# Performance work log

Hardware: AMD Instinct MI355X
Metric: run time of the kernel (lower is better)

The kernel has to match this reference:

```python
import jax, jax.numpy as jnp
import numpy as np

N = 40000          # total samples; s pattern: first N//2 are group 0, rest group 1
TOP = 0.3          # top_percentile
LAM = 10.0
ITS = 10
P = 0.5


def setup_inputs() -> dict:
    key = jax.random.key(0)
    k1, k2 = jax.random.split(key)
    y_pred = jax.random.uniform(k1, (N,), dtype=jnp.float32)  # predicted probs in [0,1]
    # deterministic half/half sensitive attribute so group sizes are static
    s = (jnp.arange(N) >= N // 2).astype(jnp.int32)
    y_gt = jax.random.uniform(k2, (N,), dtype=jnp.float32)    # unused by forward math
    pct_a = jnp.full((1,), 0.2, dtype=jnp.float32)            # unused (threshold_based=False)
    pct_b = jnp.full((1,), 0.8, dtype=jnp.float32)            # unused
    return {"y_pred": y_pred, "s": s, "y_gt": y_gt, "pct_a": pct_a, "pct_b": pct_b}


def _wasserstein(y_pred):
    n = y_pred.shape[0]
    n0 = n // 2  # s==0 count (static: s is half zeros then half ones)
    y0 = y_pred[:n0]        # s == 0 group
    y1 = y_pred[n0:]        # s == 1 group
    nc = float(n0)
    nt = float(n - n0)
    # local_reg=True, threshold_based=False -> keep top `TOP` fraction after sort
    ia0 = int((1.0 - TOP) * n0)
    ia1 = int((1.0 - TOP) * (n - n0))
    y0 = jnp.sort(y0)[ia0:]  # (m0,)
    y1 = jnp.sort(y1)[ia1:]  # (m1,)
    m0 = y0.shape[0]
    m1 = y1.shape[0]
    # sqrt(cdist(.,p=2)**2) on 1-D points == |y1_i - y0_j|
    M = jnp.abs(y1[:, None] - y0[None, :])           # (m1, m0)
    delta = jax.lax.stop_gradient(jnp.max(M))
    eff_lam = jax.lax.stop_gradient(LAM / jnp.mean(M))
    # pad with slack row/col (delta cost, 0 in corner)
    row = delta * jnp.ones((1, m0), M.dtype)
    col = jnp.concatenate([delta * jnp.ones((m1, 1), M.dtype),
                           jnp.zeros((1, 1), M.dtype)], axis=0)
    Mt = jnp.concatenate([jnp.concatenate([M, row], axis=0), col], axis=1)  # (m1+1, m0+1)
    a = jnp.concatenate([P * jnp.ones((m1, 1), M.dtype) / nt,
                         (1.0 - P) * jnp.ones((1, 1), M.dtype)], axis=0)    # (m1+1, 1)
    b = jnp.concatenate([(1.0 - P) * jnp.ones((m0, 1), M.dtype) / nc,
                         P * jnp.ones((1, 1), M.dtype)], axis=0)            # (m0+1, 1)
    K = jnp.exp(-eff_lam * Mt) + 1e-6
    ainvK = K / a
    u = a
    for _ in range(ITS):  # fixed 10-step Sinkhorn fixed point
        u = 1.0 / (ainvK @ (b / (u.T @ K).T))
    v = b / (u.T @ K).T
    T = u * (v.T * K)
    T = jax.lax.stop_gradient(T)  # backpropT=False
    D = 2.0 * jnp.sum(T * Mt)
    return D


def reference(y_pred, s, y_gt, pct_a, pct_b):
    # s is the fixed half-zeros/half-ones pattern from setup_inputs; the static
    # slices in _wasserstein reproduce the original boolean masks exactly.
    reg_loss = _wasserstein(y_pred)
    z = jnp.zeros((1,), jnp.float32)
    return (reg_loss, z, z, z)
```

## Files before the change

kernel.cpp:

```cpp
#include <hip/hip_runtime.h>

#define HALF   20000
#define MSEL   6001
#define RANKLO 13999
#define NBUCK  4096
#define CANDMAX 8192

#define NTH   1024
#define TPT   6
#define NPAD  (NTH*TPT)

#define OFF_HIST   0
#define OFF_TSEL   8192
#define OFF_CCNT   8194
#define OFF_ZERO_N 8196
#define OFF_CANDV  8704
#define OFF_CANDI  25088
#define OFF_RANK   41472
#define OFF_XS     57856
#define OFF_YS     63872

#define LPREF 0
#define LSUFB 6144
#define LCX   12288
#define LCY   18432
#define LRED  24576
#define LSC   24640
#define SOLVE_LDS_FLOATS 24656
#define SOLVE_LDS_BYTES (SOLVE_LDS_FLOATS * 4)

__device__ __forceinline__ float fexp2(float x) {
#if defined(__has_builtin)
#if __has_builtin(__builtin_amdgcn_exp2f)
  return __builtin_amdgcn_exp2f(x);
#else
  return exp2f(x);
#endif
#else
  return exp2f(x);
#endif
}

__device__ __forceinline__ int bucket_of(float v) {
  int b = (int)(v * 4096.0f);
  b = b < 0 ? 0 : b;
  b = b > (NBUCK - 1) ? (NBUCK - 1) : b;
  return b;
}


__global__ __launch_bounds__(512) void k_zero(int* wsI) {
  int i = blockIdx.x * blockDim.x + threadIdx.x;
  if (i < OFF_ZERO_N) wsI[i] = 0;
  if (i < 2 * CANDMAX) wsI[OFF_RANK + i] = 0;
}

__global__ __launch_bounds__(512) void k_hist(const float* __restrict__ yp, int* wsI) {
  int i = blockIdx.x * blockDim.x + threadIdx.x;
  if (i >= 2 * HALF) return;
  int h = (i >= HALF) ? 1 : 0;
  atomicAdd(&wsI[OFF_HIST + h * NBUCK + bucket_of(yp[i])], 1);
}

__global__ __launch_bounds__(1024) void k_findt(int* wsI) {
  __shared__ int ss[1024];
  const int h = blockIdx.x;
  const int t = threadIdx.x;
  const int* hist = wsI + OFF_HIST + h * NBUCK;
  int c0 = hist[4 * t + 0], c1 = hist[4 * t + 1], c2 = hist[4 * t + 2], c3 = hist[4 * t + 3];
  ss[t] = c0 + c1 + c2 + c3;
  __syncthreads();
  for (int off = 1; off < 1024; off <<= 1) {
    int v = ss[t];
    if (t + off < 1024) v += ss[t + off];
    __syncthreads();
    ss[t] = v;
    __syncthreads();
  }
  int SSnext = (t < 1023) ? ss[t + 1] : 0;
  int R3 = c3 + SSnext;
  int R2 = c2 + R3;
  int R1 = c1 + R2;
  int R0 = c0 + R1;
  if (R0 >= MSEL && R1 < MSEL) wsI[OFF_TSEL + h] = 4 * t + 0;
  if (R1 >= MSEL && R2 < MSEL) wsI[OFF_TSEL + h] = 4 * t + 1;
  if (R2 >= MSEL && R3 < MSEL) wsI[OFF_TSEL + h] = 4 * t + 2;
  if (R3 >= MSEL && SSnext < MSEL) wsI[OFF_TSEL + h] = 4 * t + 3;
}

__global__ __launch_bounds__(512) void k_cand(const float* __restrict__ yp, int* wsI, float* wsF) {
  __shared__ int ss[512];
  __shared__ int sbase;
  const int h = blockIdx.y;
  const int tid = threadIdx.x;
  const int idx = blockIdx.x * 512 + tid;
  float v = 0.f;
  int flag = 0;
  if (idx < HALF) {
    v = yp[h * HALF + idx];
    flag = (bucket_of(v) >= wsI[OFF_TSEL + h]) ? 1 : 0;
  }
  ss[tid] = flag;
  __syncthreads();
  for (int off = 1; off < 512; off <<= 1) {
    int add = (tid >= off) ? ss[tid - off] : 0;
    __syncthreads();
    ss[tid] += add;
    __syncthreads();
  }
  if (tid == 511) sbase = atomicAdd(&wsI[OFF_CCNT + h], ss[511]);
  __syncthreads();
  if (flag) {
    int pos = sbase + ss[tid] - 1;
    if (pos < CANDMAX) {
      wsF[OFF_CANDV + h * CANDMAX + pos] = v;
      wsI[OFF_CANDI + h * CANDMAX + pos] = idx;
    }
  }
}

__global__ __launch_bounds__(512) void k_rankc(const int* __restrict__ wsIc, float* wsF, int* wsI) {
  __shared__ float cv[512];
  __shared__ int ci[512];
  const int h = blockIdx.z;
  const int tid = threadIdx.x;
  const int cnt = min(wsIc[OFF_CCNT + h], CANDMAX);
  const int cb = blockIdx.y * 512;
  if (cb >= cnt) return;
  const int clen = min(512, cnt - cb);
  if (tid < clen) {
    cv[tid] = wsF[OFF_CANDV + h * CANDMAX + cb + tid];
    ci[tid] = wsIc[OFF_CANDI + h * CANDMAX + cb + tid];
  }
  __syncthreads();
  const int g = blockIdx.x * 512 + tid;
  if (g >= cnt) return;
  const float v = wsF[OFF_CANDV + h * CANDMAX + g];
  const int li = wsIc[OFF_CANDI + h * CANDMAX + g];
  int r = 0;
  for (int l = 0; l < clen; ++l) {
    float w = cv[l];
    r += (w < v || (w == v && ci[l] < li)) ? 1 : 0;
  }
  atomicAdd(&wsI[OFF_RANK + h * CANDMAX + g], r);
}

__global__ __launch_bounds__(512) void k_place(const int* __restrict__ wsI, float* wsF) {
  const int h = blockIdx.y;
  const int g = blockIdx.x * 512 + threadIdx.x;
  const int cnt = min(wsI[OFF_CCNT + h], CANDMAX);
  if (g >= cnt) return;
  const int full = wsI[OFF_RANK + h * CANDMAX + g] + (HALF - cnt);
  if (full >= RANKLO) {
    wsF[(h ? OFF_YS : OFF_XS) + (full - RANKLO)] = wsF[OFF_CANDV + h * CANDMAX + g];
  }
}


__device__ __forceinline__ float block_reduce(float v, float* red) {
  const int tid = threadIdx.x;
  __syncthreads();
  for (int d = 1; d < 64; d <<= 1) v += __shfl_xor(v, d, 64);
  if ((tid & 63) == 0) red[tid >> 6] = v;
  __syncthreads();
  float r = 0.f;
  if (tid < 16) {
    r = red[tid];
    for (int d = 1; d < 16; d <<= 1) r += __shfl_xor(r, d, 16);
    if (tid == 0) red[0] = r;
  }
  __syncthreads();
  return red[0];
}

__device__ __forceinline__ int bsearch(const float* arr, float v) {
  int lo = 0, hi = MSEL;
  while (lo < hi) {
    int m = (lo + hi) >> 1;
    if (arr[m] <= v) lo = m + 1; else hi = m;
  }
  return lo;
}

__device__ __forceinline__ void scan_ab(const float (&a)[TPT], const float (&b)[TPT],
                                        float wsum, float* lds,
                                        int do_state, int sout, int lout, float lnext) {
  float* PrefA = lds + LPREF;
  float* SufB = lds + LSUFB;
  float* red = lds + LRED;
  float* scal = lds + LSC;
  const int tid = threadIdx.x;
  const int wv = tid >> 6, ln = tid & 63;
  float pa[TPT], sb[TPT];
  float ta = 0.f;
#pragma unroll
  for (int k = 0; k < TPT; ++k) { pa[k] = ta; ta += a[k]; }
  float tb = 0.f;
#pragma unroll
  for (int k = TPT - 1; k >= 0; --k) { tb += b[k]; sb[k] = tb; }
  float ia = ta, ib = tb, iw = wsum;
#pragma unroll
  for (int d = 1; d < 64; d <<= 1) {
    float oa = __shfl_up(ia, d, 64);
    float ob = __shfl_down(ib, d, 64);
    float ow = __shfl_xor(iw, d, 64);
    if (ln >= d) ia += oa;
    if (ln + d < 64) ib += ob;
    iw += ow;
  }
  if (ln == 63) red[wv] = ia;
  if (ln == 0) { red[16 + wv] = ib; red[32 + wv] = iw; }
  __syncthreads();
  if (tid < 16) {
    float wa = red[tid], wb = red[16 + tid], ww = red[32 + tid];
    float sa = wa, sbw = wb, sw = ww;
#pragma unroll
    for (int d = 1; d < 16; d <<= 1) {
      float oa = __shfl_up(sa, d, 16);
      float ob = __shfl_down(sbw, d, 16);
      float ow = __shfl_xor(sw, d, 16);
      if (tid >= d) sa += oa;
      if (tid + d < 16) sbw += ob;
      sw += ow;
    }
    red[tid] = sa - wa;
    red[16 + tid] = sbw - wb;
    if (tid == 15) red[48] = sa;
    if (tid == 0) {
      red[49] = sw;
      if (do_state) { scal[sout] = sw; scal[lout] = lnext; }
    }
  }
  __syncthreads();
  const float GA = red[wv] + (ia - ta);
  const float GB = red[16 + wv] + (ib - tb);
  const int base = tid * TPT;
#pragma unroll
  for (int k = 0; k < TPT; ++k) {
    PrefA[base + k] = GA + pa[k];
    SufB[base + k] = GB + sb[k];
  }
  __syncthreads();
}

__device__ __forceinline__ void do_pass(float* lds, const float* zin, float* zout,
                                        const float (&SA)[TPT], const float (&SB)[TPT],
                                        const float (&TA)[TPT], const float (&TB)[TPT],
                                        const int (&tp)[TPT],
                                        int mode, int sin, int lin, int sout, int lout) {
  float* PrefA = lds + LPREF;
  float* SufB = lds + LSUFB;
  float* scal = lds + LSC;
  const int tid = threadIdx.x;
  const int base = tid * TPT;
  const float au = 0.5f / 20000.0f;
  const float kd = scal[2];
  float S_in = 0.f, l_in = 0.f, cin = 0.f, lnext = 0.f;
  if (mode == 1) { S_in = (float)MSEL * au; l_in = 0.5f; }
  else if (mode == 2) { S_in = scal[sin]; l_in = scal[lin]; }
  if (mode) {
    cin = 1e-6f * S_in + l_in * kd;
    lnext = 0.5f / (kd * S_in + l_in * (1.0f + 1e-6f));
  }
  float a[TPT], b[TPT];
  float wsum = 0.f;
#pragma unroll
  for (int k = 0; k < TPT; ++k) {
    int j = base + k;
    float w = 0.f;
    if (j < MSEL) w = mode ? (au / (zin[j] + cin)) : au;
    wsum += w;
    a[k] = w * SA[k];
    b[k] = w * SB[k];
  }
  scan_ab(a, b, wsum, lds, mode != 0, sout, lout, lnext);
#pragma unroll
  for (int k = 0; k < TPT; ++k) {
    int i = base + k;
    if (i < MSEL) {
      int p = tp[k];
      zout[i] = TB[k] * PrefA[p] + TA[k] * SufB[p];
    }
  }
}

__global__ __launch_bounds__(NTH) void k_solve(float* __restrict__ wsF, float* __restrict__ out) {
  extern __shared__ float lds[];
  const int tid = threadIdx.x;
  float* PrefA = lds + LPREF;
  float* SufB = lds + LSUFB;
  float* cx = lds + LCX;
  float* cy = lds + LCY;
  float* red = lds + LRED;
  float* scal = lds + LSC;
  const float au = 0.5f / 20000.0f;
  const int base = tid * TPT;

#pragma unroll
  for (int k = 0; k < TPT; ++k) {
    int j = base + k;
    cx[j] = (j < MSEL) ? wsF[OFF_XS + j] : 1e30f;
    cy[j] = (j < MSEL) ? wsF[OFF_YS + j] : 1e30f;
  }
  __syncthreads();

  float xr[TPT], yr[TPT];
  int px[TPT], py[TPT];
#pragma unroll
  for (int k = 0; k < TPT; ++k) {
    int j = base + k;
    xr[k] = (j < MSEL) ? cx[j] : 0.f;
    yr[k] = (j < MSEL) ? cy[j] : 0.f;
  }
  {
    int p = bsearch(cy, xr[0]);
    px[0] = p;
#pragma unroll
    for (int k = 1; k < TPT; ++k) {
      float x = xr[k];
      while (cy[p] <= x) ++p;
      px[k] = p;
    }
    int q = bsearch(cx, yr[0]);
    py[0] = q;
#pragma unroll
    for (int k = 1; k < TPT; ++k) {
      float y = yr[k];
      while (cx[q] <= y) ++q;
      py[k] = q;
    }
  }

  {
    float a0[TPT], b0[TPT];
#pragma unroll
    for (int k = 0; k < TPT; ++k) { a0[k] = yr[k]; b0[k] = 0.f; }
    scan_ab(a0, b0, 0.f, lds, 0, 0, 0, 0.f);
    const float PyT = red[48];
    float rs = 0.f;
#pragma unroll
    for (int k = 0; k < TPT; ++k) {
      int i = base + k;
      if (i < MSEL)
        rs += xr[k] * (float)(2 * px[k] - MSEL) + PyT - 2.f * PrefA[px[k]];
    }
    float tot = block_reduce(rs, red);
    if (tid == 0) {
      float meanM = tot / ((float)MSEL * (float)MSEL);
      float lam = 10.0f / meanM;
      float lamL2 = lam * 1.4426950408889634f;
      float delta = fmaxf(cy[MSEL - 1] - cx[0], cx[MSEL - 1] - cy[0]);
      float kd = fexp2(-lamL2 * delta) + 1e-6f;
      float lo = fminf(cx[0], cy[0]);
      float hi = fmaxf(cx[MSEL - 1], cy[MSEL - 1]);
      scal[0] = lamL2;
      scal[1] = delta;
      scal[2] = kd;
      scal[3] = 0.5f * (lo + hi);
    }
  }
  __syncthreads();

  const float lamL2 = scal[0];
  const float mid = scal[3];
  float EAx[TPT], EBx[TPT], EAy[TPT], EBy[TPT];
#pragma unroll
  for (int k = 0; k < TPT; ++k) {
    int j = base + k;
    if (j < MSEL) {
      float X = lamL2 * (xr[k] - mid);
      EAx[k] = fexp2(X);
      EBx[k] = fexp2(-X);
      float Y = lamL2 * (yr[k] - mid);
      EAy[k] = fexp2(Y);
      EBy[k] = fexp2(-Y);
    } else {
      EAx[k] = EBx[k] = EAy[k] = EBy[k] = 0.f;
    }
  }

  do_pass(lds, cx, cx, EAy, EBy, EAx, EBx, px, 0, 0, 0, 0, 0);
  for (int it = 0; it < 10; ++it) {
    do_pass(lds, cx, cy, EAx, EBx, EAy, EBy, py, (it == 0) ? 1 : 2, 5, 7, 4, 6);
    do_pass(lds, cy, cx, EAy, EBy, EAx, EBx, px, 2, 4, 6, 5, 7);
  }

  const float delta = scal[1], kd2 = scal[2];
  const float Sx = scal[4], Sy = scal[5], lX = scal[6], lY = scal[7];
  const float cin_v = 1e-6f * Sy + lY * kd2;
  const float cin_u = 1e-6f * Sx + lX * kd2;

  float v[TPT];
  float sv = 0.f, svx = 0.f;
#pragma unroll
  for (int k = 0; k < TPT; ++k) {
    int j = base + k;
    if (j < MSEL) {
      v[k] = au / (cx[j] + cin_v);
      sv += v[k];
      svx += v[k] * xr[k];
    } else v[k] = 0.f;
  }
  const float Sv = block_reduce(sv, red);
  const float TVX = block_reduce(svx, red);

  float dvk[TPT];
  float aa[TPT], bb[TPT];
#pragma unroll
  for (int k = 0; k < TPT; ++k) { aa[k] = v[k] * EAx[k]; bb[k] = v[k] * EBx[k]; }
  scan_ab(aa, bb, 0.f, lds, 0, 0, 0, 0.f);
#pragma unroll
  for (int k = 0; k < TPT; ++k) {
    int i = base + k;
    if (i < MSEL) {
      int p = py[k];
      dvk[k] = yr[k] * (EBy[k] * PrefA[p] - EAy[k] * SufB[p]);
    } else dvk[k] = 0.f;
  }
#pragma unroll
  for (int k = 0; k < TPT; ++k) { aa[k] *= xr[k]; bb[k] *= xr[k]; }
  scan_ab(aa, bb, 0.f, lds, 0, 0, 0, 0.f);
#pragma unroll
  for (int k = 0; k < TPT; ++k) {
    int i = base + k;
    if (i < MSEL) {
      int p = py[k];
      dvk[k] += -EBy[k] * PrefA[p] + EAy[k] * SufB[p];
    }
  }
#pragma unroll
  for (int k = 0; k < TPT; ++k) { aa[k] = v[k]; bb[k] = v[k] * xr[k]; }
  scan_ab(aa, bb, 0.f, lds, 0, 0, 0, 0.f);
  float acc = 0.f;
#pragma unroll
  for (int k = 0; k < TPT; ++k) {
    int i = base + k;
    if (i < MSEL) {
      int p = py[k];
      float d6 = dvk[k] + 1e-6f * (yr[k] * (2.f * PrefA[p] - Sv) + 2.f * SufB[p] - TVX);
      float u = au / (cy[i] + cin_u);
      acc += u * d6;
    }
  }
  float Dc = block_reduce(acc, red);
  if (tid == 0) {
    float v_last = 0.5f / (kd2 * Sy + lY * (1.0f + 1e-6f));
    float D = Dc + delta * kd2 * (lY * Sv + v_last * Sy);
    out[0] = 2.0f * D;
    out[1] = 0.f;
    out[2] = 0.f;
    out[3] = 0.f;
  }
}

extern "C" void kernel_launch(void* const* d_in, const int* in_sizes, int n_in,
                              void* d_out, int out_size, void* d_ws, size_t ws_size,
                              hipStream_t stream) {
  const float* yp = (const float*)d_in[0];
  float* wsF = (float*)d_ws;
  int* wsI = (int*)d_ws;
  float* out = (float*)d_out;

  k_zero<<<32, 512, 0, stream>>>(wsI);
  k_hist<<<79, 512, 0, stream>>>(yp, wsI);
  k_findt<<<2, 1024, 0, stream>>>(wsI);
  k_cand<<<dim3(40, 2), 512, 0, stream>>>(yp, wsI, wsF);
  k_rankc<<<dim3(16, 16, 2), 512, 0, stream>>>(wsI, wsF, wsI);
  k_place<<<dim3(16, 2), 512, 0, stream>>>(wsI, wsF);
  k_solve<<<1, NTH, SOLVE_LDS_BYTES, stream>>>(wsF, out);
}
```

Measured before the change: 118.1 us.

## Fuse threshold/place kernels, keep Sinkhorn state in registers, DPP scans

Folds the threshold search into k_cand and the placement step into k_solve, and replaces k_zero with a memset, removing three kernel launches. The solver now runs 768 threads with 8 elements each and keeps the Sinkhorn scaling vectors in registers instead of LDS. Block scans use DPP wave prefixes with fewer barriers, and divisions become hardware reciprocals. Reductions are folded into the existing scans. Every candidate block now recomputes the histogram scan, and the fast reciprocal can differ slightly from exact division.

```diff
diff --git a/kernel.cpp b/kernel.cpp
--- a/kernel.cpp
+++ b/kernel.cpp
@@ -6,27 +6,23 @@
 #define NBUCK  4096
 #define CANDMAX 8192
 
-#define NTH   1024
-#define TPT   6
+#define NTH   768
+#define TPT   8
 #define NPAD  (NTH*TPT)
+#define NWAVE 12
 
 #define OFF_HIST   0
-#define OFF_TSEL   8192
-#define OFF_CCNT   8194
-#define OFF_ZERO_N 8196
-#define OFF_CANDV  8704
-#define OFF_CANDI  25088
-#define OFF_RANK   41472
-#define OFF_XS     57856
-#define OFF_YS     63872
+#define OFF_CCNT   8192
+#define OFF_RANK   8704
+#define OFF_CANDV  25088
+#define OFF_CANDI  41472
+#define ZERO_BYTES (25088*4)
 
 #define LPREF 0
 #define LSUFB 6144
-#define LCX   12288
-#define LCY   18432
-#define LRED  24576
-#define LSC   24640
-#define SOLVE_LDS_FLOATS 24656
+#define LRED  12288
+#define LSC   12352
+#define SOLVE_LDS_FLOATS 12368
 #define SOLVE_LDS_BYTES (SOLVE_LDS_FLOATS * 4)
 
 __device__ __forceinline__ float fexp2(float x) {
@@ -41,6 +37,81 @@
 #endif
 }
 
+__device__ __forceinline__ float frcp(float x) {
+#if defined(__has_builtin)
+#if __has_builtin(__builtin_amdgcn_rcpf)
+  return __builtin_amdgcn_rcpf(x);
+#else
+  return 1.0f / x;
+#endif
+#else
+  return 1.0f / x;
+#endif
+}
+
+#if defined(__has_builtin)
+#if __has_builtin(__builtin_amdgcn_update_dpp) && __has_builtin(__builtin_amdgcn_readlane)
+#define HAS_DPP 1
+#endif
+#endif
+
+#ifdef HAS_DPP
+template<int CTRL, int RM>
+__device__ __forceinline__ float dppadd(float x) {
+  int s = __builtin_amdgcn_update_dpp(0, __float_as_int(x), CTRL, RM, 0xf, false);
+  return x + __int_as_float(s);
+}
+__device__ __forceinline__ float prefix64(float x) {
+  x = dppadd<0x111, 0xf>(x);
+  x = dppadd<0x112, 0xf>(x);
+  x = dppadd<0x114, 0xf>(x);
+  x = dppadd<0x118, 0xf>(x);
+  x = dppadd<0x142, 0xa>(x);
+  x = dppadd<0x143, 0xc>(x);
+  return x;
+}
+__device__ __forceinline__ float prefixrow(float x) {
+  x = dppadd<0x111, 0xf>(x);
+  x = dppadd<0x112, 0xf>(x);
+  x = dppadd<0x114, 0xf>(x);
+  x = dppadd<0x118, 0xf>(x);
+  return x;
+}
+__device__ __forceinline__ float sufrow(float x) {
+  x = dppadd<0x101, 0xf>(x);
+  x = dppadd<0x102, 0xf>(x);
+  x = dppadd<0x104, 0xf>(x);
+  x = dppadd<0x108, 0xf>(x);
+  return x;
+}
+__device__ __forceinline__ float rdlane(float x, int l) {
+  return __int_as_float(__builtin_amdgcn_readlane(__float_as_int(x), l));
+}
+#else
+__device__ __forceinline__ float prefix64(float x) {
+  for (int d = 1; d < 64; d <<= 1) {
+    float o = __shfl_up(x, d, 64);
+    if ((threadIdx.x & 63) >= d) x += o;
+  }
+  return x;
+}
+__device__ __forceinline__ float prefixrow(float x) {
+  for (int d = 1; d < 16; d <<= 1) {
+    float o = __shfl_up(x, d, 64);
+    if ((threadIdx.x & 15) >= d) x += o;
+  }
+  return x;
+}
+__device__ __forceinline__ float sufrow(float x) {
+  for (int d = 1; d < 16; d <<= 1) {
+    float o = __shfl_down(x, d, 64);
+    if ((threadIdx.x & 15) + d < 16) x += o;
+  }
+  return x;
+}
+__device__ __forceinline__ float rdlane(float x, int l) { return __shfl(x, l, 64); }
+#endif
+
 __device__ __forceinline__ int bucket_of(float v) {
   int b = (int)(v * 4096.0f);
   b = b < 0 ? 0 : b;
@@ -49,12 +120,6 @@
 }
 
 
-__global__ __launch_bounds__(512) void k_zero(int* wsI) {
-  int i = blockIdx.x * blockDim.x + threadIdx.x;
-  if (i < OFF_ZERO_N) wsI[i] = 0;
-  if (i < 2 * CANDMAX) wsI[OFF_RANK + i] = 0;
-}
-
 __global__ __launch_bounds__(512) void k_hist(const float* __restrict__ yp, int* wsI) {
   int i = blockIdx.x * blockDim.x + threadIdx.x;
   if (i >= 2 * HALF) return;
@@ -62,44 +127,50 @@
   atomicAdd(&wsI[OFF_HIST + h * NBUCK + bucket_of(yp[i])], 1);
 }
 
-__global__ __launch_bounds__(1024) void k_findt(int* wsI) {
-  __shared__ int ss[1024];
-  const int h = blockIdx.x;
-  const int t = threadIdx.x;
-  const int* hist = wsI + OFF_HIST + h * NBUCK;
-  int c0 = hist[4 * t + 0], c1 = hist[4 * t + 1], c2 = hist[4 * t + 2], c3 = hist[4 * t + 3];
-  ss[t] = c0 + c1 + c2 + c3;
-  __syncthreads();
-  for (int off = 1; off < 1024; off <<= 1) {
-    int v = ss[t];
-    if (t + off < 1024) v += ss[t + off];
-    __syncthreads();
-    ss[t] = v;
-    __syncthreads();
-  }
-  int SSnext = (t < 1023) ? ss[t + 1] : 0;
-  int R3 = c3 + SSnext;
-  int R2 = c2 + R3;
-  int R1 = c1 + R2;
-  int R0 = c0 + R1;
-  if (R0 >= MSEL && R1 < MSEL) wsI[OFF_TSEL + h] = 4 * t + 0;
-  if (R1 >= MSEL && R2 < MSEL) wsI[OFF_TSEL + h] = 4 * t + 1;
-  if (R2 >= MSEL && R3 < MSEL) wsI[OFF_TSEL + h] = 4 * t + 2;
-  if (R3 >= MSEL && SSnext < MSEL) wsI[OFF_TSEL + h] = 4 * t + 3;
-}
-
 __global__ __launch_bounds__(512) void k_cand(const float* __restrict__ yp, int* wsI, float* wsF) {
   __shared__ int ss[512];
+  __shared__ int sboundary;
   __shared__ int sbase;
   const int h = blockIdx.y;
   const int tid = threadIdx.x;
+
+  int c[8];
+  int tot = 0;
+#pragma unroll
+  for (int q = 0; q < 8; ++q) {
+    c[q] = wsI[OFF_HIST + h * NBUCK + tid * 8 + q];
+    tot += c[q];
+  }
+  if (tid == 0) sboundary = -1;
+  ss[tid] = tot;
+  __syncthreads();
+  for (int off = 1; off < 512; off <<= 1) {
+    int add = (tid >= off) ? ss[tid - off] : 0;
+    __syncthreads();
+    ss[tid] += add;
+    __syncthreads();
+  }
+  const int total = ss[511];
+  const int suffAfter = total - ss[tid];
+  int run = suffAfter;
+  int best = -1;
+#pragma unroll
+  for (int q = 7; q >= 0; --q) {
+    run += c[q];
+    if (best < 0 && run >= MSEL) best = tid * 8 + q;
+  }
+  if (best >= 0) atomicMax(&sboundary, best);
+  __syncthreads();
+  const int tsel = sboundary;
+
   const int idx = blockIdx.x * 512 + tid;
   float v = 0.f;
   int flag = 0;
   if (idx < HALF) {
     v = yp[h * HALF + idx];
-    flag = (bucket_of(v) >= wsI[OFF_TSEL + h]) ? 1 : 0;
-  }
+    flag = (bucket_of(v) >= tsel) ? 1 : 0;
+  }
+  __syncthreads();
   ss[tid] = flag;
   __syncthreads();
   for (int off = 1; off < 512; off <<= 1) {
@@ -145,17 +216,6 @@
   atomicAdd(&wsI[OFF_RANK + h * CANDMAX + g], r);
 }
 
-__global__ __launch_bounds__(512) void k_place(const int* __restrict__ wsI, float* wsF) {
-  const int h = blockIdx.y;
-  const int g = blockIdx.x * 512 + threadIdx.x;
-  const int cnt = min(wsI[OFF_CCNT + h], CANDMAX);
-  if (g >= cnt) return;
-  const int full = wsI[OFF_RANK + h * CANDMAX + g] + (HALF - cnt);
-  if (full >= RANKLO) {
-    wsF[(h ? OFF_YS : OFF_XS) + (full - RANKLO)] = wsF[OFF_CANDV + h * CANDMAX + g];
-  }
-}
-
 
 __device__ __forceinline__ float block_reduce(float v, float* red) {
   const int tid = threadIdx.x;
@@ -165,7 +225,7 @@
   __syncthreads();
   float r = 0.f;
   if (tid < 16) {
-    r = red[tid];
+    r = (tid < NWAVE) ? red[tid] : 0.f;
     for (int d = 1; d < 16; d <<= 1) r += __shfl_xor(r, d, 16);
     if (tid == 0) red[0] = r;
   }
@@ -182,13 +242,14 @@
   return lo;
 }
 
+template<bool DO_W>
 __device__ __forceinline__ void scan_ab(const float (&a)[TPT], const float (&b)[TPT],
                                         float wsum, float* lds,
-                                        int do_state, int sout, int lout, float lnext) {
+                                        int sout, int lout, float lnext) {
   float* PrefA = lds + LPREF;
-  float* SufB = lds + LSUFB;
-  float* red = lds + LRED;
-  float* scal = lds + LSC;
+  float* SufB  = lds + LSUFB;
+  float* red   = lds + LRED;
+  float* scal  = lds + LSC;
   const int tid = threadIdx.x;
   const int wv = tid >> 6, ln = tid & 63;
   float pa[TPT], sb[TPT];
@@ -198,135 +259,168 @@
   float tb = 0.f;
 #pragma unroll
   for (int k = TPT - 1; k >= 0; --k) { tb += b[k]; sb[k] = tb; }
-  float ia = ta, ib = tb, iw = wsum;
-#pragma unroll
-  for (int d = 1; d < 64; d <<= 1) {
-    float oa = __shfl_up(ia, d, 64);
-    float ob = __shfl_down(ib, d, 64);
-    float ow = __shfl_xor(iw, d, 64);
-    if (ln >= d) ia += oa;
-    if (ln + d < 64) ib += ob;
-    iw += ow;
-  }
-  if (ln == 63) red[wv] = ia;
-  if (ln == 0) { red[16 + wv] = ib; red[32 + wv] = iw; }
-  __syncthreads();
-  if (tid < 16) {
-    float wa = red[tid], wb = red[16 + tid], ww = red[32 + tid];
-    float sa = wa, sbw = wb, sw = ww;
-#pragma unroll
-    for (int d = 1; d < 16; d <<= 1) {
-      float oa = __shfl_up(sa, d, 16);
-      float ob = __shfl_down(sbw, d, 16);
-      float ow = __shfl_xor(sw, d, 16);
-      if (tid >= d) sa += oa;
-      if (tid + d < 16) sbw += ob;
-      sw += ow;
-    }
-    red[tid] = sa - wa;
-    red[16 + tid] = sbw - wb;
-    if (tid == 15) red[48] = sa;
-    if (tid == 0) {
-      red[49] = sw;
-      if (do_state) { scal[sout] = sw; scal[lout] = lnext; }
-    }
-  }
-  __syncthreads();
-  const float GA = red[wv] + (ia - ta);
-  const float GB = red[16 + wv] + (ib - tb);
+
+  float tsA = __shfl_up(ta, 1, 64);
+  if (ln == 0) tsA = 0.f;
+  const float eA = prefix64(tsA);
+  const float wTotA = rdlane(eA, 63) + rdlane(ta, 63);
+
+  float tsB = __shfl_down(tb, 1, 64);
+  if (ln == 63) tsB = 0.f;
+  const float sRow = sufrow(tsB);
+  const float r1 = rdlane(sRow, 16);
+  const float r2 = rdlane(sRow, 32);
+  const float r3 = rdlane(sRow, 48);
+  const int row = ln >> 4;
+  const float radd = (row == 0) ? (r1 + r2 + r3)
+                   : (row == 1) ? (r2 + r3)
+                   : (row == 2) ? r3 : 0.f;
+  const float eB = sRow + radd;
+  const float wTotB = rdlane(eB, 0) + rdlane(tb, 0);
+
+  float wTotW = 0.f;
+  if (DO_W) {
+    float iW = prefix64(wsum);
+    wTotW = rdlane(iW, 63);
+  }
+  if (ln == 0) {
+    red[wv] = wTotA;
+    red[16 + wv] = wTotB;
+    if (DO_W) red[32 + wv] = wTotW;
+  }
+  __syncthreads();
+  float tAs = (ln >= 1 && ln <= NWAVE) ? red[ln - 1] : 0.f;
+  const float pAe = prefixrow(tAs);
+  const float GAoff = rdlane(pAe, wv);
+  float tBr = (ln < NWAVE) ? red[16 + (NWAVE - 1 - ln)] : 0.f;
+  const float pBr = prefixrow(tBr);
+  const float GBoff = (wv < NWAVE - 1) ? rdlane(pBr, (NWAVE - 2) - wv) : 0.f;
+  if (tid == 0) {
+    red[48] = rdlane(pAe, NWAVE);
+    if (DO_W) {
+      float s = 0.f;
+#pragma unroll
+      for (int q = 0; q < NWAVE; ++q) s += red[32 + q];
+      scal[sout] = s;
+      scal[lout] = lnext;
+    }
+  }
+  const float GA = GAoff + eA;
+  const float GB = GBoff + eB;
   const int base = tid * TPT;
-#pragma unroll
-  for (int k = 0; k < TPT; ++k) {
-    PrefA[base + k] = GA + pa[k];
-    SufB[base + k] = GB + sb[k];
-  }
-  __syncthreads();
-}
-
-__device__ __forceinline__ void do_pass(float* lds, const float* zin, float* zout,
-                                        const float (&SA)[TPT], const float (&SB)[TPT],
-                                        const float (&TA)[TPT], const float (&TB)[TPT],
-                                        const int (&tp)[TPT],
-                                        int mode, int sin, int lin, int sout, int lout) {
+  float4* pp = (float4*)(PrefA + base);
+  float4* sp = (float4*)(SufB + base);
+  pp[0] = make_float4(GA + pa[0], GA + pa[1], GA + pa[2], GA + pa[3]);
+  pp[1] = make_float4(GA + pa[4], GA + pa[5], GA + pa[6], GA + pa[7]);
+  sp[0] = make_float4(GB + sb[0], GB + sb[1], GB + sb[2], GB + sb[3]);
+  sp[1] = make_float4(GB + sb[4], GB + sb[5], GB + sb[6], GB + sb[7]);
+  __syncthreads();
+}
+
+template<int MODE>
+__device__ __forceinline__ void do_pass(float* lds,
+    const float (&zin)[TPT], float (&zout)[TPT],
+    const float (&SA)[TPT], const float (&SB)[TPT],
+    const float (&TA)[TPT], const float (&TB)[TPT],
+    const int (&tp)[TPT], int sin, int lin, int sout, int lout) {
   float* PrefA = lds + LPREF;
-  float* SufB = lds + LSUFB;
-  float* scal = lds + LSC;
-  const int tid = threadIdx.x;
-  const int base = tid * TPT;
+  float* SufB  = lds + LSUFB;
+  float* scal  = lds + LSC;
+  const int base = threadIdx.x * TPT;
   const float au = 0.5f / 20000.0f;
-  const float kd = scal[2];
-  float S_in = 0.f, l_in = 0.f, cin = 0.f, lnext = 0.f;
-  if (mode == 1) { S_in = (float)MSEL * au; l_in = 0.5f; }
-  else if (mode == 2) { S_in = scal[sin]; l_in = scal[lin]; }
-  if (mode) {
+  float cin = 0.f, lnext = 0.f;
+  if (MODE) {
+    const float kd = scal[2];
+    float S_in, l_in;
+    if (MODE == 1) { S_in = (float)MSEL * au; l_in = 0.5f; }
+    else { S_in = scal[sin]; l_in = scal[lin]; }
     cin = 1e-6f * S_in + l_in * kd;
-    lnext = 0.5f / (kd * S_in + l_in * (1.0f + 1e-6f));
+    lnext = 0.5f * frcp(kd * S_in + l_in * (1.0f + 1e-6f));
   }
   float a[TPT], b[TPT];
   float wsum = 0.f;
 #pragma unroll
   for (int k = 0; k < TPT; ++k) {
-    int j = base + k;
     float w = 0.f;
-    if (j < MSEL) w = mode ? (au / (zin[j] + cin)) : au;
+    if (base + k < MSEL) w = MODE ? au * frcp(zin[k] + cin) : au;
     wsum += w;
     a[k] = w * SA[k];
     b[k] = w * SB[k];
   }
-  scan_ab(a, b, wsum, lds, mode != 0, sout, lout, lnext);
+  scan_ab<(MODE != 0)>(a, b, wsum, lds, sout, lout, lnext);
 #pragma unroll
   for (int k = 0; k < TPT; ++k) {
-    int i = base + k;
-    if (i < MSEL) {
-      int p = tp[k];
-      zout[i] = TB[k] * PrefA[p] + TA[k] * SufB[p];
-    }
-  }
-}
-
-__global__ __launch_bounds__(NTH) void k_solve(float* __restrict__ wsF, float* __restrict__ out) {
+    int p = tp[k];
+    zout[k] = (base + k < MSEL) ? (TB[k] * PrefA[p] + TA[k] * SufB[p]) : 0.f;
+  }
+}
+
+__global__ __launch_bounds__(NTH) void k_solve(const float* __restrict__ wsF,
+                                               const int* __restrict__ wsI,
+                                               float* __restrict__ out) {
   extern __shared__ float lds[];
   const int tid = threadIdx.x;
-  float* PrefA = lds + LPREF;
-  float* SufB = lds + LSUFB;
-  float* cx = lds + LCX;
-  float* cy = lds + LCY;
+  float* xs  = lds + LPREF;
+  float* ys  = lds + LSUFB;
   float* red = lds + LRED;
   float* scal = lds + LSC;
   const float au = 0.5f / 20000.0f;
   const int base = tid * TPT;
 
-#pragma unroll
-  for (int k = 0; k < TPT; ++k) {
-    int j = base + k;
-    cx[j] = (j < MSEL) ? wsF[OFF_XS + j] : 1e30f;
-    cy[j] = (j < MSEL) ? wsF[OFF_YS + j] : 1e30f;
+  {
+    float4 big = make_float4(1e30f, 1e30f, 1e30f, 1e30f);
+    ((float4*)(xs + base))[0] = big;
+    ((float4*)(xs + base))[1] = big;
+    ((float4*)(ys + base))[0] = big;
+    ((float4*)(ys + base))[1] = big;
+    if (tid < 80) lds[LRED + tid] = 0.f;
+  }
+  __syncthreads();
+  for (int h = 0; h < 2; ++h) {
+    const int cnt = min(wsI[OFF_CCNT + h], CANDMAX);
+    float* dst = h ? ys : xs;
+    for (int c = tid; c < cnt; c += NTH) {
+      int full = wsI[OFF_RANK + h * CANDMAX + c] + (HALF - cnt);
+      if (full >= RANKLO) dst[full - RANKLO] = wsF[OFF_CANDV + h * CANDMAX + c];
+    }
   }
   __syncthreads();
 
   float xr[TPT], yr[TPT];
+  {
+    float4 x0 = ((float4*)(xs + base))[0], x1 = ((float4*)(xs + base))[1];
+    float4 y0 = ((float4*)(ys + base))[0], y1 = ((float4*)(ys + base))[1];
+    float tx[TPT] = {x0.x, x0.y, x0.z, x0.w, x1.x, x1.y, x1.z, x1.w};
+    float ty[TPT] = {y0.x, y0.y, y0.z, y0.w, y1.x, y1.y, y1.z, y1.w};
+#pragma unroll
+    for (int k = 0; k < TPT; ++k) {
+      xr[k] = (base + k < MSEL) ? tx[k] : 0.f;
+      yr[k] = (base + k < MSEL) ? ty[k] : 0.f;
+    }
+  }
+  float bx0 = 0.f, bxl = 0.f, by0 = 0.f, byl = 0.f;
+  if (tid == 0) {
+    bx0 = xs[0]; bxl = xs[MSEL - 1];
+    by0 = ys[0]; byl = ys[MSEL - 1];
+  }
   int px[TPT], py[TPT];
 #pragma unroll
-  for (int k = 0; k < TPT; ++k) {
-    int j = base + k;
-    xr[k] = (j < MSEL) ? cx[j] : 0.f;
-    yr[k] = (j < MSEL) ? cy[j] : 0.f;
-  }
-  {
-    int p = bsearch(cy, xr[0]);
+  for (int k = 0; k < TPT; ++k) { px[k] = 0; py[k] = 0; }
+  if (base < MSEL) {
+    int p = bsearch(ys, xr[0]);
     px[0] = p;
 #pragma unroll
     for (int k = 1; k < TPT; ++k) {
       float x = xr[k];
-      while (cy[p] <= x) ++p;
+      while (ys[p] <= x) ++p;
       px[k] = p;
     }
-    int q = bsearch(cx, yr[0]);
+    int q = bsearch(xs, yr[0]);
     py[0] = q;
 #pragma unroll
     for (int k = 1; k < TPT; ++k) {
       float y = yr[k];
-      while (cx[q] <= y) ++q;
+      while (xs[q] <= y) ++q;
       py[k] = q;
     }
   }
@@ -335,13 +429,13 @@
     float a0[TPT], b0[TPT];
 #pragma unroll
     for (int k = 0; k < TPT; ++k) { a0[k] = yr[k]; b0[k] = 0.f; }
-    scan_ab(a0, b0, 0.f, lds, 0, 0, 0, 0.f);
+    scan_ab<false>(a0, b0, 0.f, lds, 0, 0, 0.f);
+    float* PrefA = lds + LPREF;
     const float PyT = red[48];
     float rs = 0.f;
 #pragma unroll
     for (int k = 0; k < TPT; ++k) {
-      int i = base + k;
-      if (i < MSEL)
+      if (base + k < MSEL)
         rs += xr[k] * (float)(2 * px[k] - MSEL) + PyT - 2.f * PrefA[px[k]];
     }
     float tot = block_reduce(rs, red);
@@ -349,10 +443,10 @@
       float meanM = tot / ((float)MSEL * (float)MSEL);
       float lam = 10.0f / meanM;
       float lamL2 = lam * 1.4426950408889634f;
-      float delta = fmaxf(cy[MSEL - 1] - cx[0], cx[MSEL - 1] - cy[0]);
+      float delta = fmaxf(byl - bx0, bxl - by0);
       float kd = fexp2(-lamL2 * delta) + 1e-6f;
-      float lo = fminf(cx[0], cy[0]);
-      float hi = fmaxf(cx[MSEL - 1], cy[MSEL - 1]);
+      float lo = fminf(bx0, by0);
+      float hi = fmaxf(bxl, byl);
       scal[0] = lamL2;
       scal[1] = delta;
       scal[2] = kd;
@@ -366,8 +460,7 @@
   float EAx[TPT], EBx[TPT], EAy[TPT], EBy[TPT];
 #pragma unroll
   for (int k = 0; k < TPT; ++k) {
-    int j = base + k;
-    if (j < MSEL) {
+    if (base + k < MSEL) {
       float X = lamL2 * (xr[k] - mid);
       EAx[k] = fexp2(X);
       EBx[k] = fexp2(-X);
@@ -379,66 +472,59 @@
     }
   }
 
-  do_pass(lds, cx, cx, EAy, EBy, EAx, EBx, px, 0, 0, 0, 0, 0);
-  for (int it = 0; it < 10; ++it) {
-    do_pass(lds, cx, cy, EAx, EBx, EAy, EBy, py, (it == 0) ? 1 : 2, 5, 7, 4, 6);
-    do_pass(lds, cy, cx, EAy, EBy, EAx, EBx, px, 2, 4, 6, 5, 7);
-  }
-
+  float zx[TPT], zy[TPT];
+#pragma unroll
+  for (int k = 0; k < TPT; ++k) { zx[k] = 0.f; zy[k] = 0.f; }
+  do_pass<0>(lds, zx, zx, EAy, EBy, EAx, EBx, px, 0, 0, 0, 0);
+  do_pass<1>(lds, zx, zy, EAx, EBx, EAy, EBy, py, 5, 7, 4, 6);
+  do_pass<2>(lds, zy, zx, EAy, EBy, EAx, EBx, px, 4, 6, 5, 7);
+  for (int it = 1; it < 10; ++it) {
+    do_pass<2>(lds, zx, zy, EAx, EBx, EAy, EBy, py, 5, 7, 4, 6);
+    do_pass<2>(lds, zy, zx, EAy, EBy, EAx, EBx, px, 4, 6, 5, 7);
+  }
+
+  float* PrefA = lds + LPREF;
+  float* SufB  = lds + LSUFB;
   const float delta = scal[1], kd2 = scal[2];
   const float Sx = scal[4], Sy = scal[5], lX = scal[6], lY = scal[7];
   const float cin_v = 1e-6f * Sy + lY * kd2;
   const float cin_u = 1e-6f * Sx + lX * kd2;
 
-  float v[TPT];
-  float sv = 0.f, svx = 0.f;
-#pragma unroll
-  for (int k = 0; k < TPT; ++k) {
-    int j = base + k;
-    if (j < MSEL) {
-      v[k] = au / (cx[j] + cin_v);
-      sv += v[k];
-      svx += v[k] * xr[k];
-    } else v[k] = 0.f;
-  }
-  const float Sv = block_reduce(sv, red);
-  const float TVX = block_reduce(svx, red);
+  float vv[TPT];
+#pragma unroll
+  for (int k = 0; k < TPT; ++k)
+    vv[k] = (base + k < MSEL) ? au * frcp(zx[k] + cin_v) : 0.f;
 
   float dvk[TPT];
   float aa[TPT], bb[TPT];
 #pragma unroll
-  for (int k = 0; k < TPT; ++k) { aa[k] = v[k] * EAx[k]; bb[k] = v[k] * EBx[k]; }
-  scan_ab(aa, bb, 0.f, lds, 0, 0, 0, 0.f);
+  for (int k = 0; k < TPT; ++k) { aa[k] = vv[k] * EAx[k]; bb[k] = vv[k] * EBx[k]; }
+  scan_ab<false>(aa, bb, 0.f, lds, 0, 0, 0.f);
 #pragma unroll
   for (int k = 0; k < TPT; ++k) {
-    int i = base + k;
-    if (i < MSEL) {
-      int p = py[k];
-      dvk[k] = yr[k] * (EBy[k] * PrefA[p] - EAy[k] * SufB[p]);
-    } else dvk[k] = 0.f;
-  }
-#pragma unroll
-  for (int k = 0; k < TPT; ++k) { aa[k] *= xr[k]; bb[k] *= xr[k]; }
-  scan_ab(aa, bb, 0.f, lds, 0, 0, 0, 0.f);
+    int p = py[k];
+    dvk[k] = yr[k] * (EBy[k] * PrefA[p] - EAy[k] * SufB[p]);
+  }
+#pragma unroll
+  for (int k = 0; k < TPT; ++k) { aa[k] = vv[k] * xr[k] * EAx[k]; bb[k] = vv[k] * xr[k] * EBx[k]; }
+  scan_ab<false>(aa, bb, 0.f, lds, 0, 0, 0.f);
 #pragma unroll
   for (int k = 0; k < TPT; ++k) {
-    int i = base + k;
-    if (i < MSEL) {
-      int p = py[k];
-      dvk[k] += -EBy[k] * PrefA[p] + EAy[k] * SufB[p];
-    }
-  }
-#pragma unroll
-  for (int k = 0; k < TPT; ++k) { aa[k] = v[k]; bb[k] = v[k] * xr[k]; }
-  scan_ab(aa, bb, 0.f, lds, 0, 0, 0, 0.f);
+    int p = py[k];
+    dvk[k] += -EBy[k] * PrefA[p] + EAy[k] * SufB[p];
+  }
+#pragma unroll
+  for (int k = 0; k < TPT; ++k) { aa[k] = vv[k]; bb[k] = vv[k] * xr[k]; }
+  scan_ab<false>(aa, bb, 0.f, lds, 0, 0, 0.f);
+  const float Sv = red[48];
+  const float TVX = SufB[0];
   float acc = 0.f;
 #pragma unroll
   for (int k = 0; k < TPT; ++k) {
-    int i = base + k;
-    if (i < MSEL) {
+    if (base + k < MSEL) {
       int p = py[k];
       float d6 = dvk[k] + 1e-6f * (yr[k] * (2.f * PrefA[p] - Sv) + 2.f * SufB[p] - TVX);
-      float u = au / (cy[i] + cin_u);
+      float u = au * frcp(zy[k] + cin_u);
       acc += u * d6;
     }
   }
@@ -461,11 +547,9 @@
   int* wsI = (int*)d_ws;
   float* out = (float*)d_out;
 
-  k_zero<<<32, 512, 0, stream>>>(wsI);
+  hipMemsetAsync(d_ws, 0, ZERO_BYTES, stream);
   k_hist<<<79, 512, 0, stream>>>(yp, wsI);
-  k_findt<<<2, 1024, 0, stream>>>(wsI);
   k_cand<<<dim3(40, 2), 512, 0, stream>>>(yp, wsI, wsF);
   k_rankc<<<dim3(16, 16, 2), 512, 0, stream>>>(wsI, wsF, wsI);
-  k_place<<<dim3(16, 2), 512, 0, stream>>>(wsI, wsF);
-  k_solve<<<1, NTH, SOLVE_LDS_BYTES, stream>>>(wsF, out);
-}
+  k_solve<<<1, NTH, SOLVE_LDS_BYTES, stream>>>(wsF, wsI, out);
+}
```

Result: faster. 101.7 us (-13.9%).
